# Performance work log

Measured on AMD Instinct MI355X. Metric: run time of the kernel, lower is better.

The kernel has to match this reference:

```python
import jax, jax.numpy as jnp
import numpy as np

# --- dimensions (must match init_kwargs / input_specs) ---
N = 512      # memory_size
WORD = 64    # word_size
R = 4        # num_reads
NW = 1       # num_writes
C = 512      # controller_output_size
B = 16       # batch
T = 32       # seq_len
MODES = 3    # num_read_modes
IF = R*WORD + R + NW*WORD + NW + NW*WORD + NW*WORD + R + NW + NW + R*MODES  # 471
EPS = 1e-8


def _parse_interface(v):
    # v: [B, IF] -> dict of gates/keys, mirroring _parse_interface_vector
    i = 0
    def take(n):
        nonlocal i
        s = v[:, i:i+n]
        i += n
        return s
    read_keys = take(R*WORD).reshape(-1, R, WORD)
    read_strengths = jax.nn.softplus(take(R))
    write_keys = take(NW*WORD).reshape(-1, NW, WORD)
    write_strengths = jax.nn.softplus(take(NW))
    erase_vectors = jax.nn.sigmoid(take(NW*WORD)).reshape(-1, NW, WORD)
    write_vectors = take(NW*WORD).reshape(-1, NW, WORD)
    free_gates = jax.nn.sigmoid(take(R))
    allocation_gates = jax.nn.sigmoid(take(NW))
    write_gates = jax.nn.sigmoid(take(NW))
    read_modes = jax.nn.softmax(take(R*MODES).reshape(-1, R, MODES), axis=-1)
    return dict(read_keys=read_keys, read_strengths=read_strengths,
                write_keys=write_keys, write_strengths=write_strengths,
                erase_vectors=erase_vectors, write_vectors=write_vectors,
                free_gates=free_gates, allocation_gates=allocation_gates,
                write_gates=write_gates, read_modes=read_modes)


def _content_weights(keys, strengths, memory):
    # cosine content addressing: keys [B,H,WORD], memory [B,N,WORD] -> [B,H,N]
    kn = keys * jax.lax.rsqrt(jnp.sum(keys*keys, -1, keepdims=True) + EPS)
    mn = memory * jax.lax.rsqrt(jnp.sum(memory*memory, -1, keepdims=True) + EPS)
    sim = jnp.einsum('bhw,bnw->bhn', kn, mn)
    return jax.nn.softmax(sim * strengths[..., None], axis=-1)


def _allocation(usage):
    # usage [B,N] -> allocation weighting [B,N] (DNC usage-sorted free-list)
    idx = jnp.argsort(usage, axis=-1)                      # ascending usage
    sorted_u = jnp.take_along_axis(usage, idx, axis=-1)
    cp = jnp.cumprod(sorted_u, axis=-1)
    excl = jnp.concatenate([jnp.ones_like(cp[:, :1]), cp[:, :-1]], axis=-1)
    a_sorted = (1.0 - sorted_u) * excl
    inv = jnp.argsort(idx, axis=-1)                        # unsort
    return jnp.take_along_axis(a_sorted, inv, axis=-1)


def _forward(controller_output, W_if, b_if):
    eye = jnp.eye(N, dtype=controller_output.dtype)

    def step(carry, ctrl_t):
        memory, rw, ww, link, prec, usage = carry
        p = _parse_interface(ctrl_t @ W_if + b_if)
        # write weights: content + allocation, gated
        wcw = _content_weights(p['write_keys'], p['write_strengths'], memory)  # [B,NW,N]
        alloc = _allocation(usage)[:, None, :]
        ag = p['allocation_gates'][..., None]
        wg = p['write_gates'][..., None]
        new_ww = wg * (ag * alloc + (1.0 - ag) * wcw)                           # [B,NW,N]
        # usage update (write bump then free-gate retention)
        ww_agg = 1.0 - jnp.prod(1.0 - new_ww, axis=1)                           # [B,N]
        u = usage + ww_agg - usage * ww_agg
        psi = jnp.prod(1.0 - p['free_gates'][..., None] * rw, axis=1)           # [B,N]
        new_usage = u * psi
        # memory erase + write
        erase_term = jnp.prod(1.0 - new_ww[:, :, :, None] * p['erase_vectors'][:, :, None, :], axis=1)
        new_mem = memory * erase_term + jnp.einsum('bhn,bhw->bnw', new_ww, p['write_vectors'])
        # temporal linkage (write heads summed as in the source)
        wsum = jnp.sum(new_ww, axis=1)                                          # [B,N]
        new_link = (1.0 - wsum[:, :, None] - wsum[:, None, :]) * link \
                   + wsum[:, :, None] * prec[:, None, :]
        new_link = new_link * (1.0 - eye)
        new_prec = (1.0 - jnp.sum(wsum, axis=-1, keepdims=True)) * prec + wsum
        # read weights: backward / content / forward modes
        rcw = _content_weights(p['read_keys'], p['read_strengths'], new_mem)    # [B,R,N]
        fwd = jnp.einsum('bij,brj->bri', new_link, rw)
        bwd = jnp.einsum('bji,brj->bri', new_link, rw)
        m = p['read_modes']
        new_rw = m[..., 0:1] * bwd + m[..., 1:2] * rcw + m[..., 2:3] * fwd      # [B,R,N]
        read_words = jnp.einsum('brn,bnw->brw', new_rw, new_mem)                # [B,R,WORD]
        return (new_mem, new_rw, new_ww, new_link, new_prec, new_usage), read_words

    dt = controller_output.dtype
    init = (jnp.zeros((B, N, WORD), dt),
            jnp.full((B, R, N), 1.0 / N, dt),
            jnp.full((B, NW, N), 1.0 / N, dt),
            jnp.zeros((B, N, N), dt),
            jnp.zeros((B, N), dt),
            jnp.zeros((B, N), dt))
    _, rws = jax.lax.scan(step, init, jnp.swapaxes(controller_output, 0, 1))
    return jnp.swapaxes(rws, 0, 1)  # [B,T,R,WORD]


def setup_inputs() -> dict:
    key = jax.random.key(0)
    k1, k2 = jax.random.split(key)
    controller_output = jax.random.normal(k1, (B, T, C), dtype=jnp.float32)
    W_if = jax.random.normal(k2, (C, IF), dtype=jnp.float32) * 0.05  # keep gates unsaturated
    b_if = jnp.zeros((IF,), dtype=jnp.float32)
    return {"controller_output": controller_output, "W_if": W_if, "b_if": b_if}


def reference(controller_output, W_if, b_if):
    return _forward(controller_output, W_if, b_if)
```

## Files before the change

kernel.cpp:

```cpp
#include <hip/hip_runtime.h>

#define NC 512
#define WSZ 64
#define RH 4
#define BA 16
#define TS 32
#define IFSZ 471
#define EPSC 1e-8f

__device__ __forceinline__ float wave_sum(float v) {
#pragma unroll
  for (int m = 32; m >= 1; m >>= 1) v += __shfl_xor(v, m, 64);
  return v;
}
__device__ __forceinline__ float wave_max(float v) {
#pragma unroll
  for (int m = 32; m >= 1; m >>= 1) v = fmaxf(v, __shfl_xor(v, m, 64));
  return v;
}
__device__ __forceinline__ float block_sum(float v, float* s_red, int tid) {
  float w = wave_sum(v);
  if ((tid & 63) == 0) s_red[tid >> 6] = w;
  __syncthreads();
  float tot = 0.f;
#pragma unroll
  for (int i = 0; i < 8; i++) tot += s_red[i];
  __syncthreads();
  return tot;
}
__device__ __forceinline__ float softplus_f(float x) {
  return fmaxf(x, 0.f) + log1pf(expf(-fabsf(x)));
}
__device__ __forceinline__ float sigmoid_f(float x) {
  return 1.f / (1.f + expf(-x));
}

__global__ void init_kernel(float* link, float* mem, float* us, float* pr,
                            float* ppb, float* rwi, float* wcwi) {
  size_t i = (size_t)blockIdx.x * blockDim.x + threadIdx.x;
  size_t stride = (size_t)gridDim.x * blockDim.x;
  for (size_t x = i; x < (size_t)BA * NC * NC; x += stride) link[x] = 0.f;
  for (size_t x = i; x < (size_t)BA * NC * WSZ; x += stride) mem[x] = 0.f;
  for (size_t x = i; x < (size_t)BA * RH * NC; x += stride) rwi[x] = 1.f / NC;
  for (size_t x = i; x < (size_t)BA * NC; x += stride) {
    us[x] = 0.f; pr[x] = 0.f; wcwi[x] = 1.f / NC;
  }
  for (size_t x = i; x < (size_t)16 * BA * NC; x += stride) {
    int s = (int)(x / (BA * NC));
    int n = (int)(x % NC);
    ppb[x] = (n > 32 * s) ? 0.f : 1.f;
  }
}

__global__ __launch_bounds__(512) void iface_kernel(
    const float* __restrict__ ctrl, const float* __restrict__ W,
    const float* __restrict__ bif, float* __restrict__ iface) {
  int bt = blockIdx.x;
  int tid = threadIdx.x;
  __shared__ float s_ctrl[512];
  __shared__ float s_v[IFSZ];
  s_ctrl[tid] = ctrl[(size_t)bt * 512 + tid];
  __syncthreads();
  if (tid < IFSZ) {
    float acc = bif[tid];
#pragma unroll 8
    for (int k = 0; k < 512; k++) acc = fmaf(s_ctrl[k], W[(size_t)k * IFSZ + tid], acc);
    s_v[tid] = acc;
  }
  __syncthreads();
  if (tid < IFSZ) {
    float v = s_v[tid];
    float o;
    if (tid < 256) o = v;
    else if (tid < 260) o = softplus_f(v);
    else if (tid < 324) o = v;
    else if (tid < 325) o = softplus_f(v);
    else if (tid < 389) o = sigmoid_f(v);
    else if (tid < 453) o = v;
    else if (tid < 459) o = sigmoid_f(v);
    else {
      int g = (tid - 459) / 3;
      int base = 459 + g * 3;
      float a = s_v[base], b = s_v[base + 1], c = s_v[base + 2];
      float mx = fmaxf(a, fmaxf(b, c));
      float ea = expf(a - mx), eb = expf(b - mx), ec = expf(c - mx);
      o = expf(v - mx) / (ea + eb + ec);
    }
    iface[(size_t)bt * IFSZ + tid] = o;
  }
}

__global__ __launch_bounds__(512) void fused_step(
    const float* __restrict__ iface,
    const float* __restrict__ mem_cur, float* __restrict__ mem_nxt,
    const float* __restrict__ us_old, float* __restrict__ us_new,
    const float* __restrict__ pr_old, float* __restrict__ pr_new,
    const float* __restrict__ ppb_old, float* __restrict__ ppb_new,
    const float* __restrict__ fwd_old, float* __restrict__ fwd_new,
    const float* __restrict__ bwd_old, float* __restrict__ bwd_new,
    const float* __restrict__ rw_init, const float* __restrict__ wcw_init,
    float* __restrict__ link, float* __restrict__ out, int t) {
  const int stripe = blockIdx.x, b = blockIdx.y;
  const int tid = threadIdx.x, lane = tid & 63, wid = tid >> 6;
  const int n = tid;
  const size_t bn = (size_t)b * NC;
  const float* ifcA = iface + ((size_t)b * TS + t) * IFSZ;

  __shared__ float s_rw4[4][NC];
  __shared__ float s_ww[NC], s_prec[NC], s_unew[NC];
  __shared__ float s_bpB[4][4][NC];
  __shared__ float s_keys[5][64];
  __shared__ float s_e[64], s_v[64];
  __shared__ float s_red[8];
  __shared__ float s_red5[8][5];
  __shared__ float s_part[8][4][64];

  float wcw;
  if (t > 0) {
    const float* ifcB = ifcA - IFSZ;
    if (wid < 4) {
      float k = ifcB[wid * 64 + lane];
      float ss = wave_sum(k * k);
      s_keys[wid][lane] = k * rsqrtf(ss + EPSC);
    } else if (wid == 4) {
      float k = ifcA[260 + lane];
      float ss = wave_sum(k * k);
      s_keys[4][lane] = k * rsqrtf(ss + EPSC);
    }
    __syncthreads();

    const float4* mrow = (const float4*)(mem_cur + (bn + n) * WSZ);
    float msum = 0.f, dt0 = 0.f, dt1 = 0.f, dt2 = 0.f, dt3 = 0.f, dtw = 0.f;
#pragma unroll
    for (int i = 0; i < 16; i++) {
      float4 m4 = mrow[i];
      msum = fmaf(m4.x, m4.x, fmaf(m4.y, m4.y, fmaf(m4.z, m4.z, fmaf(m4.w, m4.w, msum))));
      dt0 = fmaf(m4.x, s_keys[0][4 * i], fmaf(m4.y, s_keys[0][4 * i + 1],
            fmaf(m4.z, s_keys[0][4 * i + 2], fmaf(m4.w, s_keys[0][4 * i + 3], dt0))));
      dt1 = fmaf(m4.x, s_keys[1][4 * i], fmaf(m4.y, s_keys[1][4 * i + 1],
            fmaf(m4.z, s_keys[1][4 * i + 2], fmaf(m4.w, s_keys[1][4 * i + 3], dt1))));
      dt2 = fmaf(m4.x, s_keys[2][4 * i], fmaf(m4.y, s_keys[2][4 * i + 1],
            fmaf(m4.z, s_keys[2][4 * i + 2], fmaf(m4.w, s_keys[2][4 * i + 3], dt2))));
      dt3 = fmaf(m4.x, s_keys[3][4 * i], fmaf(m4.y, s_keys[3][4 * i + 1],
            fmaf(m4.z, s_keys[3][4 * i + 2], fmaf(m4.w, s_keys[3][4 * i + 3], dt3))));
      dtw = fmaf(m4.x, s_keys[4][4 * i], fmaf(m4.y, s_keys[4][4 * i + 1],
            fmaf(m4.z, s_keys[4][4 * i + 2], fmaf(m4.w, s_keys[4][4 * i + 3], dtw))));
    }
    float minv = rsqrtf(msum + EPSC);
    float sim[5];
    sim[0] = dt0 * minv * ifcB[256];
    sim[1] = dt1 * minv * ifcB[257];
    sim[2] = dt2 * minv * ifcB[258];
    sim[3] = dt3 * minv * ifcB[259];
    sim[4] = dtw * minv * ifcA[324];
#pragma unroll
    for (int i = 0; i < 5; i++) {
      float wm = wave_max(sim[i]);
      if (lane == 0) s_red5[wid][i] = wm;
    }
    __syncthreads();
    float ex[5];
#pragma unroll
    for (int i = 0; i < 5; i++) {
      float mx = s_red5[0][i];
#pragma unroll
      for (int w = 1; w < 8; w++) mx = fmaxf(mx, s_red5[w][i]);
      ex[i] = expf(sim[i] - mx);
    }
    __syncthreads();
#pragma unroll
    for (int i = 0; i < 5; i++) {
      float ws_ = wave_sum(ex[i]);
      if (lane == 0) s_red5[wid][i] = ws_;
    }
    __syncthreads();
    float den[5];
#pragma unroll
    for (int i = 0; i < 5; i++) {
      float s = 0.f;
#pragma unroll
      for (int w = 0; w < 8; w++) s += s_red5[w][i];
      den[i] = s;
    }
    wcw = ex[4] / den[4];
#pragma unroll
    for (int r = 0; r < 4; r++) {
      float bs = 0.f;
#pragma unroll
      for (int s = 0; s < 16; s++)
        bs += bwd_old[(((size_t)s * BA + b) * RH + r) * NC + n];
      float f = fwd_old[((size_t)b * RH + r) * NC + n];
      float rcw = ex[r] / den[r];
      float m0 = ifcB[459 + r * 3], m1 = ifcB[459 + r * 3 + 1], m2 = ifcB[459 + r * 3 + 2];
      s_rw4[r][n] = fmaf(m0, bs, fmaf(m1, rcw, m2 * f));
    }
    __syncthreads();
    if (stripe == 0) {
      float acc[4] = {0.f, 0.f, 0.f, 0.f};
      const float* mb = mem_cur + bn * WSZ;
#pragma unroll 8
      for (int k = 0; k < 64; k++) {
        int nn = wid * 64 + k;
        float m = mb[(size_t)nn * WSZ + lane];
#pragma unroll
        for (int r = 0; r < 4; r++) acc[r] = fmaf(s_rw4[r][nn], m, acc[r]);
      }
#pragma unroll
      for (int r = 0; r < 4; r++) s_part[wid][r][lane] = acc[r];
      __syncthreads();
      if (tid < 256) {
        int r = tid >> 6, w = tid & 63;
        float a = 0.f;
#pragma unroll
        for (int wv = 0; wv < 8; wv++) a += s_part[wv][r][w];
        out[(((size_t)b * TS + (t - 1)) * RH + r) * WSZ + w] = a;
      }
    }
  } else {
#pragma unroll
    for (int r = 0; r < 4; r++) s_rw4[r][n] = rw_init[((size_t)b * RH + r) * NC + n];
    wcw = wcw_init[bn + n];
    __syncthreads();
  }

  if (wid == 0) s_e[lane] = ifcA[325 + lane];
  else if (wid == 1) s_v[lane] = ifcA[389 + lane];

  float u_n = us_old[bn + n];
  float pp = 1.f;
#pragma unroll
  for (int s = 0; s < 16; s++) pp *= ppb_old[((size_t)s * BA + b) * NC + n];
  float allocv = (1.f - u_n) * pp;
  float ag = ifcA[457], wg = ifcA[458];
  float wwn = wg * (ag * allocv + (1.f - ag) * wcw);
  s_ww[n] = wwn;
  s_prec[n] = pr_old[bn + n];
  __syncthreads();

  const int i0 = stripe * 32 + wid * 4;
  float wsi[4], rwi[4][4];
#pragma unroll
  for (int rr = 0; rr < 4; rr++) {
    wsi[rr] = s_ww[i0 + rr];
#pragma unroll
    for (int r = 0; r < 4; r++) rwi[rr][r] = s_rw4[r][i0 + rr];
  }
  float facc[4][4];
  float bc[4][8];
#pragma unroll
  for (int a = 0; a < 4; a++)
#pragma unroll
    for (int c = 0; c < 4; c++) facc[a][c] = 0.f;
#pragma unroll
  for (int a = 0; a < 4; a++)
#pragma unroll
    for (int c = 0; c < 8; c++) bc[a][c] = 0.f;

  float* lbase = link + (size_t)b * NC * NC;
#pragma unroll
  for (int jj = 0; jj < 8; jj++) {
    int j = jj * 64 + lane;
    float swj = s_ww[j], spj = s_prec[j];
    float srw0 = s_rw4[0][j], srw1 = s_rw4[1][j], srw2 = s_rw4[2][j], srw3 = s_rw4[3][j];
#pragma unroll
    for (int rr = 0; rr < 4; rr++) {
      float* lp = lbase + (size_t)(i0 + rr) * NC + j;
      float l = *lp;
      float ln = fmaf(1.f - wsi[rr] - swj, l, wsi[rr] * spj);
      if (j == i0 + rr) ln = 0.f;
      *lp = ln;
      facc[rr][0] = fmaf(ln, srw0, facc[rr][0]);
      facc[rr][1] = fmaf(ln, srw1, facc[rr][1]);
      facc[rr][2] = fmaf(ln, srw2, facc[rr][2]);
      facc[rr][3] = fmaf(ln, srw3, facc[rr][3]);
      bc[0][jj] = fmaf(ln, rwi[rr][0], bc[0][jj]);
      bc[1][jj] = fmaf(ln, rwi[rr][1], bc[1][jj]);
      bc[2][jj] = fmaf(ln, rwi[rr][2], bc[2][jj]);
      bc[3][jj] = fmaf(ln, rwi[rr][3], bc[3][jj]);
    }
  }
#pragma unroll
  for (int rr = 0; rr < 4; rr++) {
#pragma unroll
    for (int r = 0; r < 4; r++) facc[rr][r] = wave_sum(facc[rr][r]);
    if (lane == 0) {
#pragma unroll
      for (int r = 0; r < 4; r++)
        fwd_new[((size_t)b * RH + r) * NC + (i0 + rr)] = facc[rr][r];
    }
  }
  if (wid >= 4) {
#pragma unroll
    for (int r = 0; r < 4; r++)
#pragma unroll
      for (int jj = 0; jj < 8; jj++) s_bpB[wid - 4][r][jj * 64 + lane] = bc[r][jj];
  }
  __syncthreads();
  if (wid < 4) {
#pragma unroll
    for (int r = 0; r < 4; r++)
#pragma unroll
      for (int jj = 0; jj < 8; jj++) s_bpB[wid][r][jj * 64 + lane] += bc[r][jj];
  }
  __syncthreads();
#pragma unroll
  for (int r = 0; r < 4; r++) {
    float a = (s_bpB[0][r][tid] + s_bpB[1][r][tid]) + (s_bpB[2][r][tid] + s_bpB[3][r][tid]);
    bwd_new[(((size_t)stripe * BA + b) * RH + r) * NC + tid] = a;
  }

  {
    const float* mob = mem_cur + bn * WSZ + (size_t)stripe * 32 * WSZ;
    float* mnb = mem_nxt + bn * WSZ + (size_t)stripe * 32 * WSZ;
#pragma unroll
    for (int kk = 0; kk < 4; kk++) {
      int flat = tid + kk * 512;
      int nn = stripe * 32 + (flat >> 6), w = flat & 63;
      mnb[flat] = fmaf(mob[flat], 1.f - s_ww[nn] * s_e[w], s_ww[nn] * s_v[w]);
    }
  }

  float u = u_n + wwn - u_n * wwn;
  float psi = 1.f;
#pragma unroll
  for (int r = 0; r < 4; r++) psi *= (1.f - ifcA[453 + r] * s_rw4[r][n]);
  float unew = u * psi;
  s_unew[n] = unew;
  __syncthreads();

  {
    float p = 1.f;
    int base = stripe * 32;
#pragma unroll
    for (int jj = 0; jj < 32; jj++) {
      int j = base + jj;
      float uj = s_unew[j];
      bool take = (uj < unew) || (uj == unew && j < n);
      p *= take ? uj : 1.f;
    }
    ppb_new[((size_t)stripe * BA + b) * NC + n] = p;
  }
  if (stripe == 15) {
    us_new[bn + n] = unew;
    float sw = block_sum(wwn, s_red, tid);
    pr_new[bn + n] = (1.f - sw) * s_prec[n] + wwn;
  }
}

__global__ __launch_bounds__(512) void final_read(
    const float* __restrict__ iface, const float* __restrict__ mem_cur,
    const float* __restrict__ fwd_old, const float* __restrict__ bwd_old,
    float* __restrict__ out) {
  const int r = blockIdx.x, b = blockIdx.y;
  const int tid = threadIdx.x, lane = tid & 63, wid = tid >> 6;
  const int n = tid;
  const int t = TS - 1;
  const size_t bn = (size_t)b * NC;
  const float* ifc = iface + ((size_t)b * TS + t) * IFSZ;
  __shared__ float s_k[64];
  __shared__ float s_rw[NC];
  __shared__ float s_part[8][64];
  __shared__ float s_red[8];

  if (wid == 0) {
    float k = ifc[r * 64 + lane];
    float ss = wave_sum(k * k);
    s_k[lane] = k * rsqrtf(ss + EPSC);
  }
  __syncthreads();

  const float4* mrow = (const float4*)(mem_cur + (bn + n) * WSZ);
  float msum = 0.f, dot = 0.f;
#pragma unroll
  for (int i = 0; i < 16; i++) {
    float4 m4 = mrow[i];
    msum = fmaf(m4.x, m4.x, fmaf(m4.y, m4.y, fmaf(m4.z, m4.z, fmaf(m4.w, m4.w, msum))));
    dot = fmaf(m4.x, s_k[4 * i], fmaf(m4.y, s_k[4 * i + 1],
          fmaf(m4.z, s_k[4 * i + 2], fmaf(m4.w, s_k[4 * i + 3], dot))));
  }
  float sim = dot * rsqrtf(msum + EPSC) * ifc[256 + r];
  float wm = wave_max(sim);
  if (lane == 0) s_red[wid] = wm;
  __syncthreads();
  float mx = s_red[0];
#pragma unroll
  for (int i = 1; i < 8; i++) mx = fmaxf(mx, s_red[i]);
  __syncthreads();
  float e = expf(sim - mx);
  float ssum = block_sum(e, s_red, tid);
  float rcw = e / ssum;
  float bs = 0.f;
#pragma unroll
  for (int s = 0; s < 16; s++)
    bs += bwd_old[(((size_t)s * BA + b) * RH + r) * NC + n];
  float f = fwd_old[((size_t)b * RH + r) * NC + n];
  float m0 = ifc[459 + r * 3], m1 = ifc[459 + r * 3 + 1], m2 = ifc[459 + r * 3 + 2];
  s_rw[n] = fmaf(m0, bs, fmaf(m1, rcw, m2 * f));
  __syncthreads();

  float acc = 0.f;
  const float* mb = mem_cur + bn * WSZ;
#pragma unroll 8
  for (int k = 0; k < 64; k++) {
    int nn = wid * 64 + k;
    acc = fmaf(s_rw[nn], mb[(size_t)nn * WSZ + lane], acc);
  }
  s_part[wid][lane] = acc;
  __syncthreads();
  if (tid < 64) {
    float a = 0.f;
#pragma unroll
    for (int w = 0; w < 8; w++) a += s_part[w][tid];
    out[(((size_t)b * TS + t) * RH + r) * WSZ + tid] = a;
  }
}

extern "C" void kernel_launch(void* const* d_in, const int* in_sizes, int n_in,
                              void* d_out, int out_size, void* d_ws, size_t ws_size,
                              hipStream_t stream) {
  const float* ctrl = (const float*)d_in[0];
  const float* Wif = (const float*)d_in[1];
  const float* bif = (const float*)d_in[2];
  float* out = (float*)d_out;

  float* p = (float*)d_ws;
  float* link = p;    p += (size_t)BA * NC * NC;
  float* mem0 = p;    p += (size_t)BA * NC * WSZ;
  float* mem1 = p;    p += (size_t)BA * NC * WSZ;
  float* iface = p;   p += (size_t)BA * TS * IFSZ;
  float* us0 = p;     p += (size_t)BA * NC;
  float* us1 = p;     p += (size_t)BA * NC;
  float* pr0 = p;     p += (size_t)BA * NC;
  float* pr1 = p;     p += (size_t)BA * NC;
  float* ppb0 = p;    p += (size_t)16 * BA * NC;
  float* ppb1 = p;    p += (size_t)16 * BA * NC;
  float* fwd0 = p;    p += (size_t)BA * RH * NC;
  float* fwd1 = p;    p += (size_t)BA * RH * NC;
  float* bwd0 = p;    p += (size_t)16 * BA * RH * NC;
  float* bwd1 = p;    p += (size_t)16 * BA * RH * NC;
  float* rwi = p;     p += (size_t)BA * RH * NC;
  float* wcwi = p;    p += (size_t)BA * NC;

  float* mem[2] = {mem0, mem1};
  float* us[2] = {us0, us1};
  float* pr[2] = {pr0, pr1};
  float* ppb[2] = {ppb0, ppb1};
  float* fwd[2] = {fwd0, fwd1};
  float* bwd[2] = {bwd0, bwd1};

  hipLaunchKernelGGL(init_kernel, dim3(2048), dim3(256), 0, stream,
                     link, mem0, us0, pr0, ppb0, rwi, wcwi);
  hipLaunchKernelGGL(iface_kernel, dim3(BA * TS), dim3(512), 0, stream,
                     ctrl, Wif, bif, iface);
  for (int t = 0; t < TS; t++) {
    int cp = t & 1, cq = cp ^ 1;
    hipLaunchKernelGGL(fused_step, dim3(16, BA), dim3(512), 0, stream,
                       iface, mem[cp], mem[cq], us[cp], us[cq], pr[cp], pr[cq],
                       ppb[cp], ppb[cq], fwd[cp], fwd[cq], bwd[cp], bwd[cq],
                       rwi, wcwi, link, out, t);
  }
  hipLaunchKernelGGL(final_read, dim3(RH, BA), dim3(512), 0, stream,
                     iface, mem[0], fwd[0], bwd[0], out);
}
```

Before: 1.166 ms.

## Transpose partial buffers, distribute read across stripes, prefetch link and memory into registers

Stores the per-stripe partial products (ppb, bwd) with the stripe index innermost so each consumer reads them with four float4 loads instead of sixteen strided loads. The read-vector computation, previously done only by stripe 0 over all 512 rows, is split so each stripe computes a partial over its own 32 rows into a new opT buffer, which the next step or final_read sums. Link rows, memory rows and other state are loaded into registers at kernel start to overlap global latency with the key setup, some barriers are merged, and launch bounds now request two blocks per CU. This adds register pressure and an extra buffer, and the output is written one step late.

Result: slower. 1.931 ms (+65.6%).

```diff
diff --git a/kernel.cpp b/kernel.cpp
--- a/kernel.cpp
+++ b/kernel.cpp
@@ -36,7 +36,7 @@
 }
 
 __global__ void init_kernel(float* link, float* mem, float* us, float* pr,
-                            float* ppb, float* rwi, float* wcwi) {
+                            float* ppbT, float* rwi, float* wcwi) {
   size_t i = (size_t)blockIdx.x * blockDim.x + threadIdx.x;
   size_t stride = (size_t)gridDim.x * blockDim.x;
   for (size_t x = i; x < (size_t)BA * NC * NC; x += stride) link[x] = 0.f;
@@ -45,10 +45,10 @@
   for (size_t x = i; x < (size_t)BA * NC; x += stride) {
     us[x] = 0.f; pr[x] = 0.f; wcwi[x] = 1.f / NC;
   }
-  for (size_t x = i; x < (size_t)16 * BA * NC; x += stride) {
-    int s = (int)(x / (BA * NC));
-    int n = (int)(x % NC);
-    ppb[x] = (n > 32 * s) ? 0.f : 1.f;
+  for (size_t x = i; x < (size_t)BA * NC * 16; x += stride) {
+    int rem = (int)(x % (NC * 16));
+    int n = rem >> 4, s = rem & 15;
+    ppbT[x] = (n > 32 * s) ? 0.f : 1.f;
   }
 }
 
@@ -90,14 +90,15 @@
   }
 }
 
-__global__ __launch_bounds__(512) void fused_step(
+__global__ __launch_bounds__(512, 2) void fused_step(
     const float* __restrict__ iface,
     const float* __restrict__ mem_cur, float* __restrict__ mem_nxt,
     const float* __restrict__ us_old, float* __restrict__ us_new,
     const float* __restrict__ pr_old, float* __restrict__ pr_new,
-    const float* __restrict__ ppb_old, float* __restrict__ ppb_new,
+    const float* __restrict__ ppbT_old, float* __restrict__ ppbT_new,
     const float* __restrict__ fwd_old, float* __restrict__ fwd_new,
-    const float* __restrict__ bwd_old, float* __restrict__ bwd_new,
+    const float* __restrict__ bwdT_old, float* __restrict__ bwdT_new,
+    const float* __restrict__ opT_old, float* __restrict__ opT_new,
     const float* __restrict__ rw_init, const float* __restrict__ wcw_init,
     float* __restrict__ link, float* __restrict__ out, int t) {
   const int stripe = blockIdx.x, b = blockIdx.y;
@@ -105,73 +106,127 @@
   const int n = tid;
   const size_t bn = (size_t)b * NC;
   const float* ifcA = iface + ((size_t)b * TS + t) * IFSZ;
-
+  const float* ifcB = ifcA - IFSZ;
+
+  __shared__ float s_keys[5][64];
+  __shared__ float s_e[64], s_v[64];
   __shared__ float s_rw4[4][NC];
   __shared__ float s_ww[NC], s_prec[NC], s_unew[NC];
+  __shared__ float s_redA[8][5], s_redB[8][5];
+  __shared__ float s_part[8][4][64];
   __shared__ float s_bpB[4][4][NC];
-  __shared__ float s_keys[5][64];
-  __shared__ float s_e[64], s_v[64];
   __shared__ float s_red[8];
-  __shared__ float s_red5[8][5];
-  __shared__ float s_part[8][4][64];
-
+
+  if (stripe == 1 && t >= 2 && tid < 256) {
+    int r = tid >> 6, w = tid & 63;
+    const float4* q = (const float4*)&opT_old[(((size_t)b * RH + r) * WSZ + w) * 16];
+    float4 a0 = q[0], a1 = q[1], a2 = q[2], a3 = q[3];
+    float s = a0.x + a0.y + a0.z + a0.w;
+    s += a1.x + a1.y + a1.z + a1.w;
+    s += a2.x + a2.y + a2.z + a2.w;
+    s += a3.x + a3.y + a3.z + a3.w;
+    out[(((size_t)b * TS + (t - 2)) * RH + r) * WSZ + w] = s;
+  }
+
+  const int i0 = stripe * 32 + wid * 4;
+  float* lbase = link + (size_t)b * NC * NC;
+  float lreg[4][8];
+#pragma unroll
+  for (int rr = 0; rr < 4; rr++)
+#pragma unroll
+    for (int jj = 0; jj < 8; jj++)
+      lreg[rr][jj] = lbase[(size_t)(i0 + rr) * NC + jj * 64 + lane];
+
+  float mo4[4];
+  {
+    const float* ms = mem_cur + bn * WSZ + (size_t)stripe * 32 * WSZ;
+#pragma unroll
+    for (int kk = 0; kk < 4; kk++) mo4[kk] = ms[tid + kk * 512];
+  }
+  float u_n = us_old[bn + n];
+  float pr_n = pr_old[bn + n];
+  float4 ppq0, ppq1, ppq2, ppq3;
+  {
+    const float4* q = (const float4*)&ppbT_old[(bn + n) * 16];
+    ppq0 = q[0]; ppq1 = q[1]; ppq2 = q[2]; ppq3 = q[3];
+  }
+
+  if (t > 0 && wid < 4) {
+    float k = ifcB[wid * 64 + lane];
+    float ss = wave_sum(k * k);
+    s_keys[wid][lane] = k * rsqrtf(ss + EPSC);
+  } else if (t > 0 && wid == 4) {
+    float k = ifcA[260 + lane];
+    float ss = wave_sum(k * k);
+    s_keys[4][lane] = k * rsqrtf(ss + EPSC);
+  } else if (wid == 5) {
+    s_e[lane] = ifcA[325 + lane];
+  } else if (wid == 6) {
+    s_v[lane] = ifcA[389 + lane];
+  }
+
+  float4 m4[16];
+  float4 bq[4][4];
+  float f4[4];
+  float rwreg[4];
   float wcw;
   if (t > 0) {
-    const float* ifcB = ifcA - IFSZ;
-    if (wid < 4) {
-      float k = ifcB[wid * 64 + lane];
-      float ss = wave_sum(k * k);
-      s_keys[wid][lane] = k * rsqrtf(ss + EPSC);
-    } else if (wid == 4) {
-      float k = ifcA[260 + lane];
-      float ss = wave_sum(k * k);
-      s_keys[4][lane] = k * rsqrtf(ss + EPSC);
-    }
-    __syncthreads();
-
     const float4* mrow = (const float4*)(mem_cur + (bn + n) * WSZ);
-    float msum = 0.f, dt0 = 0.f, dt1 = 0.f, dt2 = 0.f, dt3 = 0.f, dtw = 0.f;
+#pragma unroll
+    for (int i = 0; i < 16; i++) m4[i] = mrow[i];
+#pragma unroll
+    for (int r = 0; r < 4; r++) {
+      const float4* q = (const float4*)&bwdT_old[(((size_t)b * RH + r) * NC + n) * 16];
+#pragma unroll
+      for (int qq = 0; qq < 4; qq++) bq[r][qq] = q[qq];
+      f4[r] = fwd_old[((size_t)b * RH + r) * NC + n];
+    }
+  } else {
+#pragma unroll
+    for (int r = 0; r < 4; r++) rwreg[r] = rw_init[((size_t)b * RH + r) * NC + n];
+    wcw = wcw_init[bn + n];
+  }
+  __syncthreads();
+
+  if (t > 0) {
+    float msum = 0.f, d0 = 0.f, d1 = 0.f, d2 = 0.f, d3 = 0.f, dw = 0.f;
 #pragma unroll
     for (int i = 0; i < 16; i++) {
-      float4 m4 = mrow[i];
-      msum = fmaf(m4.x, m4.x, fmaf(m4.y, m4.y, fmaf(m4.z, m4.z, fmaf(m4.w, m4.w, msum))));
-      dt0 = fmaf(m4.x, s_keys[0][4 * i], fmaf(m4.y, s_keys[0][4 * i + 1],
-            fmaf(m4.z, s_keys[0][4 * i + 2], fmaf(m4.w, s_keys[0][4 * i + 3], dt0))));
-      dt1 = fmaf(m4.x, s_keys[1][4 * i], fmaf(m4.y, s_keys[1][4 * i + 1],
-            fmaf(m4.z, s_keys[1][4 * i + 2], fmaf(m4.w, s_keys[1][4 * i + 3], dt1))));
-      dt2 = fmaf(m4.x, s_keys[2][4 * i], fmaf(m4.y, s_keys[2][4 * i + 1],
-            fmaf(m4.z, s_keys[2][4 * i + 2], fmaf(m4.w, s_keys[2][4 * i + 3], dt2))));
-      dt3 = fmaf(m4.x, s_keys[3][4 * i], fmaf(m4.y, s_keys[3][4 * i + 1],
-            fmaf(m4.z, s_keys[3][4 * i + 2], fmaf(m4.w, s_keys[3][4 * i + 3], dt3))));
-      dtw = fmaf(m4.x, s_keys[4][4 * i], fmaf(m4.y, s_keys[4][4 * i + 1],
-            fmaf(m4.z, s_keys[4][4 * i + 2], fmaf(m4.w, s_keys[4][4 * i + 3], dtw))));
+      float4 mm = m4[i];
+      msum = fmaf(mm.x, mm.x, fmaf(mm.y, mm.y, fmaf(mm.z, mm.z, fmaf(mm.w, mm.w, msum))));
+      d0 = fmaf(mm.x, s_keys[0][4 * i], fmaf(mm.y, s_keys[0][4 * i + 1],
+           fmaf(mm.z, s_keys[0][4 * i + 2], fmaf(mm.w, s_keys[0][4 * i + 3], d0))));
+      d1 = fmaf(mm.x, s_keys[1][4 * i], fmaf(mm.y, s_keys[1][4 * i + 1],
+           fmaf(mm.z, s_keys[1][4 * i + 2], fmaf(mm.w, s_keys[1][4 * i + 3], d1))));
+      d2 = fmaf(mm.x, s_keys[2][4 * i], fmaf(mm.y, s_keys[2][4 * i + 1],
+           fmaf(mm.z, s_keys[2][4 * i + 2], fmaf(mm.w, s_keys[2][4 * i + 3], d2))));
+      d3 = fmaf(mm.x, s_keys[3][4 * i], fmaf(mm.y, s_keys[3][4 * i + 1],
+           fmaf(mm.z, s_keys[3][4 * i + 2], fmaf(mm.w, s_keys[3][4 * i + 3], d3))));
+      dw = fmaf(mm.x, s_keys[4][4 * i], fmaf(mm.y, s_keys[4][4 * i + 1],
+           fmaf(mm.z, s_keys[4][4 * i + 2], fmaf(mm.w, s_keys[4][4 * i + 3], dw))));
     }
     float minv = rsqrtf(msum + EPSC);
     float sim[5];
-    sim[0] = dt0 * minv * ifcB[256];
-    sim[1] = dt1 * minv * ifcB[257];
-    sim[2] = dt2 * minv * ifcB[258];
-    sim[3] = dt3 * minv * ifcB[259];
-    sim[4] = dtw * minv * ifcA[324];
+    sim[0] = d0 * minv * ifcB[256];
+    sim[1] = d1 * minv * ifcB[257];
+    sim[2] = d2 * minv * ifcB[258];
+    sim[3] = d3 * minv * ifcB[259];
+    sim[4] = dw * minv * ifcA[324];
 #pragma unroll
     for (int i = 0; i < 5; i++) {
       float wm = wave_max(sim[i]);
-      if (lane == 0) s_red5[wid][i] = wm;
+      if (lane == 0) s_redA[wid][i] = wm;
     }
     __syncthreads();
     float ex[5];
 #pragma unroll
     for (int i = 0; i < 5; i++) {
-      float mx = s_red5[0][i];
-#pragma unroll
-      for (int w = 1; w < 8; w++) mx = fmaxf(mx, s_red5[w][i]);
+      float mx = s_redA[0][i];
+#pragma unroll
+      for (int w = 1; w < 8; w++) mx = fmaxf(mx, s_redA[w][i]);
       ex[i] = expf(sim[i] - mx);
-    }
-    __syncthreads();
-#pragma unroll
-    for (int i = 0; i < 5; i++) {
       float ws_ = wave_sum(ex[i]);
-      if (lane == 0) s_red5[wid][i] = ws_;
+      if (lane == 0) s_redB[wid][i] = ws_;
     }
     __syncthreads();
     float den[5];
@@ -179,71 +234,64 @@
     for (int i = 0; i < 5; i++) {
       float s = 0.f;
 #pragma unroll
-      for (int w = 0; w < 8; w++) s += s_red5[w][i];
+      for (int w = 0; w < 8; w++) s += s_redB[w][i];
       den[i] = s;
     }
     wcw = ex[4] / den[4];
 #pragma unroll
     for (int r = 0; r < 4; r++) {
-      float bs = 0.f;
-#pragma unroll
-      for (int s = 0; s < 16; s++)
-        bs += bwd_old[(((size_t)s * BA + b) * RH + r) * NC + n];
-      float f = fwd_old[((size_t)b * RH + r) * NC + n];
+      float bs = bq[r][0].x + bq[r][0].y + bq[r][0].z + bq[r][0].w;
+      bs += bq[r][1].x + bq[r][1].y + bq[r][1].z + bq[r][1].w;
+      bs += bq[r][2].x + bq[r][2].y + bq[r][2].z + bq[r][2].w;
+      bs += bq[r][3].x + bq[r][3].y + bq[r][3].z + bq[r][3].w;
       float rcw = ex[r] / den[r];
       float m0 = ifcB[459 + r * 3], m1 = ifcB[459 + r * 3 + 1], m2 = ifcB[459 + r * 3 + 2];
-      s_rw4[r][n] = fmaf(m0, bs, fmaf(m1, rcw, m2 * f));
-    }
-    __syncthreads();
-    if (stripe == 0) {
-      float acc[4] = {0.f, 0.f, 0.f, 0.f};
-      const float* mb = mem_cur + bn * WSZ;
-#pragma unroll 8
-      for (int k = 0; k < 64; k++) {
-        int nn = wid * 64 + k;
-        float m = mb[(size_t)nn * WSZ + lane];
-#pragma unroll
-        for (int r = 0; r < 4; r++) acc[r] = fmaf(s_rw4[r][nn], m, acc[r]);
-      }
-#pragma unroll
-      for (int r = 0; r < 4; r++) s_part[wid][r][lane] = acc[r];
-      __syncthreads();
-      if (tid < 256) {
-        int r = tid >> 6, w = tid & 63;
-        float a = 0.f;
-#pragma unroll
-        for (int wv = 0; wv < 8; wv++) a += s_part[wv][r][w];
-        out[(((size_t)b * TS + (t - 1)) * RH + r) * WSZ + w] = a;
-      }
-    }
-  } else {
-#pragma unroll
-    for (int r = 0; r < 4; r++) s_rw4[r][n] = rw_init[((size_t)b * RH + r) * NC + n];
-    wcw = wcw_init[bn + n];
-    __syncthreads();
-  }
-
-  if (wid == 0) s_e[lane] = ifcA[325 + lane];
-  else if (wid == 1) s_v[lane] = ifcA[389 + lane];
-
-  float u_n = us_old[bn + n];
-  float pp = 1.f;
-#pragma unroll
-  for (int s = 0; s < 16; s++) pp *= ppb_old[((size_t)s * BA + b) * NC + n];
+      rwreg[r] = fmaf(m0, bs, fmaf(m1, rcw, m2 * f4[r]));
+    }
+  }
+
+#pragma unroll
+  for (int r = 0; r < 4; r++) s_rw4[r][n] = rwreg[r];
+  float pp = ppq0.x * ppq0.y * ppq0.z * ppq0.w;
+  pp *= ppq1.x * ppq1.y * ppq1.z * ppq1.w;
+  pp *= ppq2.x * ppq2.y * ppq2.z * ppq2.w;
+  pp *= ppq3.x * ppq3.y * ppq3.z * ppq3.w;
   float allocv = (1.f - u_n) * pp;
   float ag = ifcA[457], wg = ifcA[458];
   float wwn = wg * (ag * allocv + (1.f - ag) * wcw);
   s_ww[n] = wwn;
-  s_prec[n] = pr_old[bn + n];
-  __syncthreads();
-
-  const int i0 = stripe * 32 + wid * 4;
-  float wsi[4], rwi[4][4];
+  s_prec[n] = pr_n;
+  float u = u_n + wwn - u_n * wwn;
+  float psi = 1.f;
+#pragma unroll
+  for (int r = 0; r < 4; r++) psi *= (1.f - ifcA[453 + r] * rwreg[r]);
+  float unew = u * psi;
+  s_unew[n] = unew;
+  __syncthreads();
+
+  if (t > 0) {
+    float p0 = 0.f, p1 = 0.f, p2 = 0.f, p3 = 0.f;
+#pragma unroll
+    for (int kk = 0; kk < 4; kk++) {
+      int row = stripe * 32 + wid + kk * 8;
+      float m = mo4[kk];
+      p0 = fmaf(s_rw4[0][row], m, p0);
+      p1 = fmaf(s_rw4[1][row], m, p1);
+      p2 = fmaf(s_rw4[2][row], m, p2);
+      p3 = fmaf(s_rw4[3][row], m, p3);
+    }
+    s_part[wid][0][lane] = p0;
+    s_part[wid][1][lane] = p1;
+    s_part[wid][2][lane] = p2;
+    s_part[wid][3][lane] = p3;
+  }
+
+  float wsi[4], rwi4[4][4];
 #pragma unroll
   for (int rr = 0; rr < 4; rr++) {
     wsi[rr] = s_ww[i0 + rr];
 #pragma unroll
-    for (int r = 0; r < 4; r++) rwi[rr][r] = s_rw4[r][i0 + rr];
+    for (int r = 0; r < 4; r++) rwi4[rr][r] = s_rw4[r][i0 + rr];
   }
   float facc[4][4];
   float bc[4][8];
@@ -256,7 +304,6 @@
 #pragma unroll
     for (int c = 0; c < 8; c++) bc[a][c] = 0.f;
 
-  float* lbase = link + (size_t)b * NC * NC;
 #pragma unroll
   for (int jj = 0; jj < 8; jj++) {
     int j = jj * 64 + lane;
@@ -264,19 +311,17 @@
     float srw0 = s_rw4[0][j], srw1 = s_rw4[1][j], srw2 = s_rw4[2][j], srw3 = s_rw4[3][j];
 #pragma unroll
     for (int rr = 0; rr < 4; rr++) {
-      float* lp = lbase + (size_t)(i0 + rr) * NC + j;
-      float l = *lp;
-      float ln = fmaf(1.f - wsi[rr] - swj, l, wsi[rr] * spj);
+      float ln = fmaf(1.f - wsi[rr] - swj, lreg[rr][jj], wsi[rr] * spj);
       if (j == i0 + rr) ln = 0.f;
-      *lp = ln;
+      lbase[(size_t)(i0 + rr) * NC + j] = ln;
       facc[rr][0] = fmaf(ln, srw0, facc[rr][0]);
       facc[rr][1] = fmaf(ln, srw1, facc[rr][1]);
       facc[rr][2] = fmaf(ln, srw2, facc[rr][2]);
       facc[rr][3] = fmaf(ln, srw3, facc[rr][3]);
-      bc[0][jj] = fmaf(ln, rwi[rr][0], bc[0][jj]);
-      bc[1][jj] = fmaf(ln, rwi[rr][1], bc[1][jj]);
-      bc[2][jj] = fmaf(ln, rwi[rr][2], bc[2][jj]);
-      bc[3][jj] = fmaf(ln, rwi[rr][3], bc[3][jj]);
+      bc[0][jj] = fmaf(ln, rwi4[rr][0], bc[0][jj]);
+      bc[1][jj] = fmaf(ln, rwi4[rr][1], bc[1][jj]);
+      bc[2][jj] = fmaf(ln, rwi4[rr][2], bc[2][jj]);
+      bc[3][jj] = fmaf(ln, rwi4[rr][3], bc[3][jj]);
     }
   }
 #pragma unroll
@@ -306,51 +351,47 @@
 #pragma unroll
   for (int r = 0; r < 4; r++) {
     float a = (s_bpB[0][r][tid] + s_bpB[1][r][tid]) + (s_bpB[2][r][tid] + s_bpB[3][r][tid]);
-    bwd_new[(((size_t)stripe * BA + b) * RH + r) * NC + tid] = a;
-  }
-
+    bwdT_new[(((size_t)b * RH + r) * NC + tid) * 16 + stripe] = a;
+  }
+  if (t > 0 && tid < 256) {
+    int r = tid >> 6, w = tid & 63;
+    float a = 0.f;
+#pragma unroll
+    for (int wv = 0; wv < 8; wv++) a += s_part[wv][r][w];
+    opT_new[(((size_t)b * RH + r) * WSZ + w) * 16 + stripe] = a;
+  }
   {
-    const float* mob = mem_cur + bn * WSZ + (size_t)stripe * 32 * WSZ;
     float* mnb = mem_nxt + bn * WSZ + (size_t)stripe * 32 * WSZ;
 #pragma unroll
     for (int kk = 0; kk < 4; kk++) {
       int flat = tid + kk * 512;
-      int nn = stripe * 32 + (flat >> 6), w = flat & 63;
-      mnb[flat] = fmaf(mob[flat], 1.f - s_ww[nn] * s_e[w], s_ww[nn] * s_v[w]);
-    }
-  }
-
-  float u = u_n + wwn - u_n * wwn;
-  float psi = 1.f;
-#pragma unroll
-  for (int r = 0; r < 4; r++) psi *= (1.f - ifcA[453 + r] * s_rw4[r][n]);
-  float unew = u * psi;
-  s_unew[n] = unew;
-  __syncthreads();
-
+      int row = stripe * 32 + wid + kk * 8;
+      mnb[flat] = fmaf(mo4[kk], 1.f - s_ww[row] * s_e[lane], s_ww[row] * s_v[lane]);
+    }
+  }
   {
-    float p = 1.f;
-    int base = stripe * 32;
+    float pslice = 1.f;
+    int base0 = stripe * 32;
 #pragma unroll
     for (int jj = 0; jj < 32; jj++) {
-      int j = base + jj;
+      int j = base0 + jj;
       float uj = s_unew[j];
       bool take = (uj < unew) || (uj == unew && j < n);
-      p *= take ? uj : 1.f;
-    }
-    ppb_new[((size_t)stripe * BA + b) * NC + n] = p;
+      pslice *= take ? uj : 1.f;
+    }
+    ppbT_new[(bn + n) * 16 + stripe] = pslice;
   }
   if (stripe == 15) {
     us_new[bn + n] = unew;
     float sw = block_sum(wwn, s_red, tid);
-    pr_new[bn + n] = (1.f - sw) * s_prec[n] + wwn;
+    pr_new[bn + n] = (1.f - sw) * pr_n + wwn;
   }
 }
 
 __global__ __launch_bounds__(512) void final_read(
     const float* __restrict__ iface, const float* __restrict__ mem_cur,
-    const float* __restrict__ fwd_old, const float* __restrict__ bwd_old,
-    float* __restrict__ out) {
+    const float* __restrict__ fwd_old, const float* __restrict__ bwdT_old,
+    const float* __restrict__ opT_old, float* __restrict__ out) {
   const int r = blockIdx.x, b = blockIdx.y;
   const int tid = threadIdx.x, lane = tid & 63, wid = tid >> 6;
   const int n = tid;
@@ -362,6 +403,17 @@
   __shared__ float s_part[8][64];
   __shared__ float s_red[8];
 
+  if (r == 0 && tid < 256) {
+    int rr = tid >> 6, w = tid & 63;
+    const float4* q = (const float4*)&opT_old[(((size_t)b * RH + rr) * WSZ + w) * 16];
+    float4 a0 = q[0], a1 = q[1], a2 = q[2], a3 = q[3];
+    float s = a0.x + a0.y + a0.z + a0.w;
+    s += a1.x + a1.y + a1.z + a1.w;
+    s += a2.x + a2.y + a2.z + a2.w;
+    s += a3.x + a3.y + a3.z + a3.w;
+    out[(((size_t)b * TS + (TS - 2)) * RH + rr) * WSZ + w] = s;
+  }
+
   if (wid == 0) {
     float k = ifc[r * 64 + lane];
     float ss = wave_sum(k * k);
@@ -390,9 +442,14 @@
   float ssum = block_sum(e, s_red, tid);
   float rcw = e / ssum;
   float bs = 0.f;
-#pragma unroll
-  for (int s = 0; s < 16; s++)
-    bs += bwd_old[(((size_t)s * BA + b) * RH + r) * NC + n];
+  {
+    const float4* q = (const float4*)&bwdT_old[(((size_t)b * RH + r) * NC + n) * 16];
+    float4 a0 = q[0], a1 = q[1], a2 = q[2], a3 = q[3];
+    bs = a0.x + a0.y + a0.z + a0.w;
+    bs += a1.x + a1.y + a1.z + a1.w;
+    bs += a2.x + a2.y + a2.z + a2.w;
+    bs += a3.x + a3.y + a3.z + a3.w;
+  }
   float f = fwd_old[((size_t)b * RH + r) * NC + n];
   float m0 = ifc[459 + r * 3], m1 = ifc[459 + r * 3 + 1], m2 = ifc[459 + r * 3 + 2];
   s_rw[n] = fmaf(m0, bs, fmaf(m1, rcw, m2 * f));
@@ -432,33 +489,36 @@
   float* us1 = p;     p += (size_t)BA * NC;
   float* pr0 = p;     p += (size_t)BA * NC;
   float* pr1 = p;     p += (size_t)BA * NC;
-  float* ppb0 = p;    p += (size_t)16 * BA * NC;
-  float* ppb1 = p;    p += (size_t)16 * BA * NC;
+  float* ppbT0 = p;   p += (size_t)BA * NC * 16;
+  float* ppbT1 = p;   p += (size_t)BA * NC * 16;
   float* fwd0 = p;    p += (size_t)BA * RH * NC;
   float* fwd1 = p;    p += (size_t)BA * RH * NC;
-  float* bwd0 = p;    p += (size_t)16 * BA * RH * NC;
-  float* bwd1 = p;    p += (size_t)16 * BA * RH * NC;
+  float* bwdT0 = p;   p += (size_t)BA * RH * NC * 16;
+  float* bwdT1 = p;   p += (size_t)BA * RH * NC * 16;
+  float* opT0 = p;    p += (size_t)BA * RH * WSZ * 16;
+  float* opT1 = p;    p += (size_t)BA * RH * WSZ * 16;
   float* rwi = p;     p += (size_t)BA * RH * NC;
   float* wcwi = p;    p += (size_t)BA * NC;
 
   float* mem[2] = {mem0, mem1};
   float* us[2] = {us0, us1};
   float* pr[2] = {pr0, pr1};
-  float* ppb[2] = {ppb0, ppb1};
+  float* ppbT[2] = {ppbT0, ppbT1};
   float* fwd[2] = {fwd0, fwd1};
-  float* bwd[2] = {bwd0, bwd1};
+  float* bwdT[2] = {bwdT0, bwdT1};
+  float* opT[2] = {opT0, opT1};
 
   hipLaunchKernelGGL(init_kernel, dim3(2048), dim3(256), 0, stream,
-                     link, mem0, us0, pr0, ppb0, rwi, wcwi);
+                     link, mem0, us0, pr0, ppbT0, rwi, wcwi);
   hipLaunchKernelGGL(iface_kernel, dim3(BA * TS), dim3(512), 0, stream,
                      ctrl, Wif, bif, iface);
   for (int t = 0; t < TS; t++) {
-    int cp = t & 1, cq = cp ^ 1;
+    int rd = t & 1, wr = rd ^ 1;
     hipLaunchKernelGGL(fused_step, dim3(16, BA), dim3(512), 0, stream,
-                       iface, mem[cp], mem[cq], us[cp], us[cq], pr[cp], pr[cq],
-                       ppb[cp], ppb[cq], fwd[cp], fwd[cq], bwd[cp], bwd[cq],
-                       rwi, wcwi, link, out, t);
+                       iface, mem[rd], mem[wr], us[rd], us[wr], pr[rd], pr[wr],
+                       ppbT[rd], ppbT[wr], fwd[rd], fwd[wr], bwdT[rd], bwdT[wr],
+                       opT[rd], opT[wr], rwi, wcwi, link, out, t);
   }
   hipLaunchKernelGGL(final_read, dim3(RH, BA), dim3(512), 0, stream,
-                     iface, mem[0], fwd[0], bwd[0], out);
-}
+                     iface, mem[0], fwd[0], bwdT[0], opT[0], out);
+}
```
